# Optimization experiments

Measured on AMD Instinct MI355X. Metric: run time of the kernel, lower is better.

Reference implementation:

```python
import jax, jax.numpy as jnp
import numpy as np

B, N, HID = 8, 1024, 768
HEADS, LORA, HDIM = 12, 256, 64


def setup_inputs() -> dict:
    key = jax.random.key(0)
    k1, k2, k3 = jax.random.split(key, 3)
    hidden_states = jax.random.normal(k1, (B, N, HID), dtype=jnp.float32)
    attention_mask = jnp.ones((B, N), dtype=jnp.int32)
    # torch Linear weights are [out_features, in_features]
    Wt = jax.random.normal(k2, (HEADS, LORA, HID), dtype=jnp.float32) * (HID ** -0.5)
    Wa = jax.random.normal(k3, (HEADS, HDIM, LORA), dtype=jnp.float32) * (LORA ** -0.5)
    return {"hidden_states": hidden_states, "attention_mask": attention_mask,
            "Wt": Wt, "Wa": Wa}


def reference(hidden_states, attention_mask, Wt, Wa):
    # Per-head LoRA projection, batched over heads instead of a Python loop.
    # t: [b, h, n, head_dim]; repeat(1,1,3) in the original makes q = k = v = t.
    scale = hidden_states.shape[-1] ** -0.5  # input_dim ** -0.5
    t = jnp.einsum('bnd,hld->bhnl', hidden_states, Wt)
    t = jnp.einsum('bhnl,hel->bhne', t, Wa)
    scores = jnp.einsum('bhid,bhjd->bhij', t, t) * scale
    scores = jnp.where(attention_mask[:, None, None, :] == 0, -jnp.inf, scores)
    attn = jax.nn.softmax(scores, axis=-1)
    out = jnp.einsum('bhij,bhjd->bhid', attn, t)  # [b, h, n, d]
    b, h, n, d = out.shape
    return out.transpose(0, 2, 1, 3).reshape(b, n, h * d)
```

## Files before the change

### kernel.cpp

```cpp
#include <hip/hip_runtime.h>
#include <math.h>

#define BATCH 8
#define SEQ   1024
#define HID_  768
#define HEADS 12
#define LORA  256
#define HDIM  64

#define SCALE      0.03608439182435161f
#define SCALE_LOG2 0.05205863235888918f

typedef _Float16 f16_t;
typedef _Float16 f16x2 __attribute__((ext_vector_type(2)));
typedef _Float16 f16x4 __attribute__((ext_vector_type(4)));
typedef _Float16 f16x8 __attribute__((ext_vector_type(8)));
typedef float    f32x4 __attribute__((ext_vector_type(4)));

#define GLD16(g, l) __builtin_amdgcn_global_load_lds( \
    (const __attribute__((address_space(1))) void*)(g), \
    (__attribute__((address_space(3))) void*)(l), 16, 0, 0)

#define SW(c, r) ((((c) ^ ((r) & 7)) << 3))

#define N4_HS (BATCH * SEQ * HID_ / 4)

__global__ __launch_bounds__(256) void cvt_hs_kernel(
    const float4* __restrict__ hs, f16x4* __restrict__ hs_f)
{
    int stride = gridDim.x * blockDim.x;
    for (int i = blockIdx.x * blockDim.x + threadIdx.x; i < N4_HS; i += stride) {
        float4 v = hs[i];
        f16x4 o = {(f16_t)v.x, (f16_t)v.y, (f16_t)v.z, (f16_t)v.w};
        hs_f[i] = o;
    }
}

__global__ __launch_bounds__(256) void fuse_w_kernel(
    const float* __restrict__ Wt, const float* __restrict__ Wa,
    f16_t* __restrict__ w_f)
{
    __shared__ float s_a[64][68];
    __shared__ float s_b[64][36];

    const int bid = blockIdx.x;
    const int h   = bid / 24;
    const int d0  = (bid % 24) * 32;
    const int tid = threadIdx.x;
    const int ty  = tid >> 4;
    const int tx  = tid & 15;

    const float* wa_g = Wa + (size_t)h * HDIM * LORA;
    const float* wt_g = Wt + (size_t)h * LORA * HID_;

    float acc[4][2] = {{0.f, 0.f}, {0.f, 0.f}, {0.f, 0.f}, {0.f, 0.f}};

    for (int kc = 0; kc < 4; ++kc) {
        const int l0 = kc * 64;
        if (kc) __syncthreads();
        #pragma unroll
        for (int k = 0; k < 4; ++k) {
            int u = tid + k * 256;
            int r = u >> 4, c4 = (u & 15) * 4;
            *(float4*)&s_a[r][c4] = *(const float4*)&wa_g[(size_t)r * LORA + l0 + c4];
        }
        #pragma unroll
        for (int k = 0; k < 2; ++k) {
            int u = tid + k * 256;
            int r = u >> 3, c4 = (u & 7) * 4;
            *(float4*)&s_b[r][c4] = *(const float4*)&wt_g[(size_t)(l0 + r) * HID_ + d0 + c4];
        }
        __syncthreads();

        #pragma unroll 8
        for (int l = 0; l < 64; ++l) {
            float a0 = s_a[ty * 4 + 0][l];
            float a1 = s_a[ty * 4 + 1][l];
            float a2 = s_a[ty * 4 + 2][l];
            float a3 = s_a[ty * 4 + 3][l];
            float b0 = s_b[l][tx * 2 + 0];
            float b1 = s_b[l][tx * 2 + 1];
            acc[0][0] = fmaf(a0, b0, acc[0][0]); acc[0][1] = fmaf(a0, b1, acc[0][1]);
            acc[1][0] = fmaf(a1, b0, acc[1][0]); acc[1][1] = fmaf(a1, b1, acc[1][1]);
            acc[2][0] = fmaf(a2, b0, acc[2][0]); acc[2][1] = fmaf(a2, b1, acc[2][1]);
            acc[3][0] = fmaf(a3, b0, acc[3][0]); acc[3][1] = fmaf(a3, b1, acc[3][1]);
        }
    }

    f16_t* wg = w_f + (size_t)h * HDIM * HID_;
    #pragma unroll
    for (int i = 0; i < 4; ++i) {
        int e = ty * 4 + i;
        f16x2 o = {(f16_t)acc[i][0], (f16_t)acc[i][1]};
        *(f16x2*)&wg[(size_t)e * HID_ + d0 + tx * 2] = o;
    }
}

__global__ __launch_bounds__(256, 3) void gemm_t(
    const f16_t* __restrict__ hs_f, const f16_t* __restrict__ w_f,
    f16_t* __restrict__ t_f, f16_t* __restrict__ tT_f)
{
    __shared__ __attribute__((aligned(16))) char smem[49152];
    f16_t* s_hs = (f16_t*)smem;
    f16_t* s_wt = (f16_t*)(smem + 32768);
    f16_t* s_ob = (f16_t*)smem;

    const int bid   = blockIdx.x;
    const int ntile = bid & 7;
    const int h     = (bid >> 3) % HEADS;
    const int b     = bid / (8 * HEADS);
    const int n0    = ntile * 128;
    const int tid   = threadIdx.x;
    const int w     = tid >> 6;
    const int lane  = tid & 63;
    const int q     = lane >> 4;
    const int mr    = lane & 15;
    const int lrow  = lane >> 3;
    const int gswz  = (((lane & 7) ^ lrow) & 7) * 8;

    const f16_t* hs_g = hs_f + ((size_t)b * SEQ + n0) * HID_;
    const f16_t* w_g  = w_f + (size_t)h * HDIM * HID_;

    const f32x4 z4 = {0.f, 0.f, 0.f, 0.f};
    f32x4 acc[2][4];
    #pragma unroll
    for (int mt = 0; mt < 2; ++mt)
        #pragma unroll
        for (int et = 0; et < 4; ++et) acc[mt][et] = z4;

    auto STAGE = [&](int buf, int rd) {
        const int k0 = rd * 64;
        f16_t* sa = s_hs + buf * (128 * 64);
        f16_t* sb = s_wt + buf * (64 * 64);
        #pragma unroll
        for (int tt = 0; tt < 4; ++tt) {
            int r0 = w * 32 + tt * 8;
            GLD16(hs_g + (size_t)(r0 + lrow) * HID_ + k0 + gswz, sa + r0 * 64);
        }
        #pragma unroll
        for (int tt = 0; tt < 2; ++tt) {
            int r0 = w * 16 + tt * 8;
            GLD16(w_g + (size_t)(r0 + lrow) * HID_ + k0 + gswz, sb + r0 * 64);
        }
    };

    auto COMPUTE = [&](int buf) {
        const f16_t* sa = s_hs + buf * (128 * 64);
        const f16_t* sb = s_wt + buf * (64 * 64);
        #pragma unroll
        for (int ks = 0; ks < 2; ++ks) {
            f16x8 a_[2], b_[4];
            #pragma unroll
            for (int mt = 0; mt < 2; ++mt)
                a_[mt] = *(const f16x8*)(sa + (w * 32 + mt * 16 + mr) * 64 + SW(ks * 4 + q, mr));
            #pragma unroll
            for (int et = 0; et < 4; ++et)
                b_[et] = *(const f16x8*)(sb + (et * 16 + mr) * 64 + SW(ks * 4 + q, mr));
            #pragma unroll
            for (int mt = 0; mt < 2; ++mt)
                #pragma unroll
                for (int et = 0; et < 4; ++et)
                    acc[mt][et] = __builtin_amdgcn_mfma_f32_16x16x32_f16(a_[mt], b_[et], acc[mt][et], 0, 0, 0);
        }
    };

    STAGE(0, 0);
    __syncthreads();
    #pragma unroll 1
    for (int rr = 0; rr < 6; ++rr) {
        STAGE(1, 2 * rr + 1);
        COMPUTE(0);
        __syncthreads();
        if (rr < 5) STAGE(0, 2 * rr + 2);
        COMPUTE(1);
        __syncthreads();
    }

    #pragma unroll
    for (int mt = 0; mt < 2; ++mt) {
        #pragma unroll
        for (int et = 0; et < 4; ++et) {
            #pragma unroll
            for (int r = 0; r < 4; ++r) {
                int row = w * 32 + mt * 16 + q * 4 + r;
                int col = et * 16 + mr;
                s_ob[row * 72 + col] = (f16_t)acc[mt][et][r];
            }
        }
    }
    __syncthreads();

    f16_t* tg = t_f + (((size_t)b * HEADS + h) * SEQ + n0) * HDIM;
    #pragma unroll
    for (int k = 0; k < 4; ++k) {
        int u = tid + k * 256;
        int row = u >> 3, c8 = (u & 7) * 8;
        *(f16x8*)&tg[row * 64 + c8] = *(const f16x8*)&s_ob[row * 72 + c8];
    }
    f16_t* tTg = tT_f + ((size_t)b * HEADS + h) * SEQ * HDIM;
    #pragma unroll
    for (int k = 0; k < 4; ++k) {
        int u = tid + k * 256;
        int e = u & 63, n8 = (u >> 6) * 8;
        f16x8 v;
        #pragma unroll
        for (int j = 0; j < 8; ++j) v[j] = s_ob[(n8 + j) * 72 + e];
        *(f16x8*)&tTg[(size_t)e * SEQ + n0 + n8] = v;
    }
}

__global__ __launch_bounds__(256, 3) void attn_mfma(
    const f16_t* __restrict__ t_f, const f16_t* __restrict__ tT_f,
    const int* __restrict__ mask, float* __restrict__ out)
{
    __shared__ __attribute__((aligned(16))) char smem[34816];
    f16_t* s_k = (f16_t*)smem;
    f16_t* s_v = (f16_t*)(smem + 8192);
    f16_t* s_p = (f16_t*)(smem + 16384);
    float* s_m = (float*)smem;

    const int bid  = blockIdx.x;
    const int it   = bid & 7;
    const int h    = (bid >> 3) % HEADS;
    const int b    = bid / (8 * HEADS);
    const int i0   = it * 128;
    const int tid  = threadIdx.x;
    const int w    = tid >> 6;
    const int lane = tid & 63;
    const int q    = lane >> 4;
    const int mr   = lane & 15;
    const int lrow = lane >> 3;
    const int gswz = (((lane & 7) ^ lrow) & 7) * 8;
    const int ih   = w >> 1;
    const int jh   = w & 1;

    const size_t bh = ((size_t)b * HEADS + h) * SEQ * HDIM;
    const f16_t* th = t_f + bh;
    const f16_t* vh = tT_f + bh;
    const int* mk = mask + (size_t)b * SEQ;

    f16x8 qf[4][2];
    #pragma unroll
    for (int mt = 0; mt < 4; ++mt)
        #pragma unroll
        for (int ks = 0; ks < 2; ++ks) {
            f16x8 v = *(const f16x8*)(th + (size_t)(i0 + ih * 64 + mt * 16 + mr) * 64
                                      + ks * 32 + q * 8);
            #pragma unroll
            for (int j = 0; j < 8; ++j) v[j] = v[j] * (f16_t)SCALE_LOG2;
            qf[mt][ks] = v;
        }

    const f32x4 z4 = {0.f, 0.f, 0.f, 0.f};
    float l_[4] = {0.f, 0.f, 0.f, 0.f};
    f32x4 oT[4][4];
    #pragma unroll
    for (int mt = 0; mt < 4; ++mt)
        #pragma unroll
        for (int et = 0; et < 4; ++et) oT[mt][et] = z4;

    for (int jt6 = 0; jt6 < 16; ++jt6) {
        const int j0 = jt6 * 64;
        __syncthreads();
        #pragma unroll
        for (int t2 = 0; t2 < 2; ++t2) {
            int r0 = w * 16 + t2 * 8;
            GLD16(th + (size_t)(j0 + r0 + lrow) * 64 + gswz,  s_k + r0 * 64);
            GLD16(vh + (size_t)(r0 + lrow) * SEQ + j0 + gswz, s_v + r0 * 64);
        }
        __syncthreads();

        #pragma unroll
        for (int jt = 0; jt < 2; ++jt) {
            f32x4 st[4] = {z4, z4, z4, z4};
            #pragma unroll
            for (int ks = 0; ks < 2; ++ks) {
                f16x8 kf = *(const f16x8*)(s_k + (jh * 32 + jt * 16 + mr) * 64 + SW(ks * 4 + q, mr));
                #pragma unroll
                for (int mt = 0; mt < 4; ++mt)
                    st[mt] = __builtin_amdgcn_mfma_f32_16x16x32_f16(kf, qf[mt][ks], st[mt], 0, 0, 0);
            }
            int4 mv = *(const int4*)(mk + j0 + jh * 32 + jt * 16 + q * 4);
            #pragma unroll
            for (int mt = 0; mt < 4; ++mt) {
                float p0 = (mv.x == 0) ? 0.f : __builtin_amdgcn_exp2f(st[mt][0]);
                float p1 = (mv.y == 0) ? 0.f : __builtin_amdgcn_exp2f(st[mt][1]);
                float p2 = (mv.z == 0) ? 0.f : __builtin_amdgcn_exp2f(st[mt][2]);
                float p3 = (mv.w == 0) ? 0.f : __builtin_amdgcn_exp2f(st[mt][3]);
                l_[mt] += (p0 + p1) + (p2 + p3);
                f16x4 u4 = {(f16_t)p0, (f16_t)p1, (f16_t)p2, (f16_t)p3};
                *(f16x4*)&s_p[(ih * 64 + mt * 16 + mr) * 72 + jh * 32 + jt * 16 + q * 4] = u4;
            }
        }

        f16x8 pf[4];
        #pragma unroll
        for (int mt = 0; mt < 4; ++mt)
            pf[mt] = *(const f16x8*)(s_p + (ih * 64 + mt * 16 + mr) * 72 + jh * 32 + q * 8);
        #pragma unroll
        for (int et = 0; et < 4; ++et) {
            f16x8 vv = *(const f16x8*)(s_v + (et * 16 + mr) * 64 + SW(jh * 4 + q, mr));
            #pragma unroll
            for (int mt = 0; mt < 4; ++mt)
                oT[mt][et] = __builtin_amdgcn_mfma_f32_16x16x32_f16(vv, pf[mt], oT[mt][et], 0, 0, 0);
        }
    }

    #pragma unroll
    for (int mt = 0; mt < 4; ++mt) {
        l_[mt] += __shfl_xor(l_[mt], 16);
        l_[mt] += __shfl_xor(l_[mt], 32);
    }

    __syncthreads();
    if (jh == 1) {
        float* dst = s_m + ((size_t)ih * 64 + lane) * 68;
        #pragma unroll
        for (int mt = 0; mt < 4; ++mt) {
            #pragma unroll
            for (int et = 0; et < 4; ++et)
                *(f32x4*)&dst[(mt * 4 + et) * 4] = oT[mt][et];
            dst[64 + mt] = l_[mt];
        }
    }
    __syncthreads();
    if (jh == 0) {
        const float* src = s_m + ((size_t)ih * 64 + lane) * 68;
        #pragma unroll
        for (int mt = 0; mt < 4; ++mt) {
            float lt = l_[mt] + src[64 + mt];
            float inv = (lt > 0.f) ? 1.f / lt : 0.f;
            int n = i0 + ih * 64 + mt * 16 + mr;
            #pragma unroll
            for (int et = 0; et < 4; ++et) {
                f32x4 o2 = *(const f32x4*)&src[(mt * 4 + et) * 4];
                float4 v = {(oT[mt][et][0] + o2[0]) * inv, (oT[mt][et][1] + o2[1]) * inv,
                            (oT[mt][et][2] + o2[2]) * inv, (oT[mt][et][3] + o2[3]) * inv};
                *(float4*)&out[((size_t)b * SEQ + n) * (HEADS * HDIM) + h * HDIM + et * 16 + q * 4] = v;
            }
        }
    }
}

extern "C" void kernel_launch(void* const* d_in, const int* in_sizes, int n_in,
                              void* d_out, int out_size, void* d_ws, size_t ws_size,
                              hipStream_t stream) {
    const float* hs   = (const float*)d_in[0];
    const int*   mask = (const int*)d_in[1];
    const float* Wt   = (const float*)d_in[2];
    const float* Wa   = (const float*)d_in[3];
    float* out = (float*)d_out;

    char* ws = (char*)d_ws;
    f16_t* t_f  = (f16_t*)ws;
    f16_t* tT_f = (f16_t*)(ws + 12582912);
    f16_t* hs_f = (f16_t*)(ws + 25165824);
    f16_t* w_f  = (f16_t*)(ws + 37748736);

    cvt_hs_kernel<<<1024, 256, 0, stream>>>((const float4*)hs, (f16x4*)hs_f);

    fuse_w_kernel<<<HEADS * (HID_ / 32), 256, 0, stream>>>(Wt, Wa, w_f);

    gemm_t<<<BATCH * HEADS * (SEQ / 128), 256, 0, stream>>>(hs_f, w_f, t_f, tT_f);

    attn_mfma<<<BATCH * HEADS * (SEQ / 128), 256, 0, stream>>>(
        t_f, tT_f, mask, out);
}
```

Measured before the change: 157.8 us.

## Double-buffer K/V tiles in attention, merge prep kernels, swizzle P buffer

The hs conversion and weight-fusion kernels become one launch, with different blocks taking each role, which saves a launch and lets the two jobs overlap. The attention kernel now double-buffers its K/V LDS tiles, so the async global-to-LDS load of the next 64-column tile is issued before the current tile is processed, and it drops one barrier per iteration. The P staging buffer changes from padded rows to an XOR-swizzled layout, fp16 conversion uses packed cvt_pkrtz, and block order is remapped so consecutive blocks cover different batch-heads. LDS use grows from 34816 to 49152 bytes, which may limit how many blocks fit per CU. Packed round-toward-zero conversion also differs slightly in rounding from the previous casts.

```diff
diff --git a/kernel.cpp b/kernel.cpp
--- a/kernel.cpp
+++ b/kernel.cpp
@@ -25,28 +25,30 @@
 
 #define N4_HS (BATCH * SEQ * HID_ / 4)
 
-__global__ __launch_bounds__(256) void cvt_hs_kernel(
-    const float4* __restrict__ hs, f16x4* __restrict__ hs_f)
-{
-    int stride = gridDim.x * blockDim.x;
-    for (int i = blockIdx.x * blockDim.x + threadIdx.x; i < N4_HS; i += stride) {
-        float4 v = hs[i];
-        f16x4 o = {(f16_t)v.x, (f16_t)v.y, (f16_t)v.z, (f16_t)v.w};
-        hs_f[i] = o;
-    }
-}
-
-__global__ __launch_bounds__(256) void fuse_w_kernel(
-    const float* __restrict__ Wt, const float* __restrict__ Wa,
+__global__ __launch_bounds__(256) void prep_kernel(
+    const float4* __restrict__ hs, const float* __restrict__ Wt,
+    const float* __restrict__ Wa, f16x4* __restrict__ hs_f,
     f16_t* __restrict__ w_f)
 {
     __shared__ float s_a[64][68];
     __shared__ float s_b[64][36];
 
+    const int tid = threadIdx.x;
+
+    if (blockIdx.x >= 288) {
+        int i0 = (blockIdx.x - 288) * 256 + tid;
+        int stride = (gridDim.x - 288) * 256;
+        for (int i = i0; i < N4_HS; i += stride) {
+            float4 v = hs[i];
+            f16x4 o = {(f16_t)v.x, (f16_t)v.y, (f16_t)v.z, (f16_t)v.w};
+            hs_f[i] = o;
+        }
+        return;
+    }
+
     const int bid = blockIdx.x;
     const int h   = bid / 24;
     const int d0  = (bid % 24) * 32;
-    const int tid = threadIdx.x;
     const int ty  = tid >> 4;
     const int tx  = tid & 15;
 
@@ -213,16 +215,17 @@
     const f16_t* __restrict__ t_f, const f16_t* __restrict__ tT_f,
     const int* __restrict__ mask, float* __restrict__ out)
 {
-    __shared__ __attribute__((aligned(16))) char smem[34816];
+    __shared__ __attribute__((aligned(16))) char smem[49152];
     f16_t* s_k = (f16_t*)smem;
-    f16_t* s_v = (f16_t*)(smem + 8192);
-    f16_t* s_p = (f16_t*)(smem + 16384);
+    f16_t* s_v = (f16_t*)(smem + 16384);
+    f16_t* s_p = (f16_t*)(smem + 32768);
     float* s_m = (float*)smem;
 
     const int bid  = blockIdx.x;
-    const int it   = bid & 7;
-    const int h    = (bid >> 3) % HEADS;
-    const int b    = bid / (8 * HEADS);
+    const int bh   = bid % (BATCH * HEADS);
+    const int it   = bid / (BATCH * HEADS);
+    const int h    = bh % HEADS;
+    const int b    = bh / HEADS;
     const int i0   = it * 128;
     const int tid  = threadIdx.x;
     const int w    = tid >> 6;
@@ -234,9 +237,9 @@
     const int ih   = w >> 1;
     const int jh   = w & 1;
 
-    const size_t bh = ((size_t)b * HEADS + h) * SEQ * HDIM;
-    const f16_t* th = t_f + bh;
-    const f16_t* vh = tT_f + bh;
+    const size_t bh_off = ((size_t)b * HEADS + h) * SEQ * HDIM;
+    const f16_t* th = t_f + bh_off;
+    const f16_t* vh = tT_f + bh_off;
     const int* mk = mask + (size_t)b * SEQ;
 
     f16x8 qf[4][2];
@@ -259,28 +262,32 @@
         #pragma unroll
         for (int et = 0; et < 4; ++et) oT[mt][et] = z4;
 
-    for (int jt6 = 0; jt6 < 16; ++jt6) {
-        const int j0 = jt6 * 64;
-        __syncthreads();
+    auto STAGE = [&](int buf, int j0) {
+        f16_t* dk = s_k + buf * 4096;
+        f16_t* dv = s_v + buf * 4096;
         #pragma unroll
         for (int t2 = 0; t2 < 2; ++t2) {
             int r0 = w * 16 + t2 * 8;
-            GLD16(th + (size_t)(j0 + r0 + lrow) * 64 + gswz,  s_k + r0 * 64);
-            GLD16(vh + (size_t)(r0 + lrow) * SEQ + j0 + gswz, s_v + r0 * 64);
-        }
-        __syncthreads();
-
+            GLD16(th + (size_t)(j0 + r0 + lrow) * 64 + gswz,  dk + r0 * 64);
+            GLD16(vh + (size_t)(r0 + lrow) * SEQ + j0 + gswz, dv + r0 * 64);
+        }
+    };
+
+    auto PROCESS = [&](int buf, int j0) {
+        const f16_t* sk = s_k + buf * 4096;
+        const f16_t* sv = s_v + buf * 4096;
         #pragma unroll
         for (int jt = 0; jt < 2; ++jt) {
             f32x4 st[4] = {z4, z4, z4, z4};
             #pragma unroll
             for (int ks = 0; ks < 2; ++ks) {
-                f16x8 kf = *(const f16x8*)(s_k + (jh * 32 + jt * 16 + mr) * 64 + SW(ks * 4 + q, mr));
+                f16x8 kf = *(const f16x8*)(sk + (jh * 32 + jt * 16 + mr) * 64 + SW(ks * 4 + q, mr));
                 #pragma unroll
                 for (int mt = 0; mt < 4; ++mt)
                     st[mt] = __builtin_amdgcn_mfma_f32_16x16x32_f16(kf, qf[mt][ks], st[mt], 0, 0, 0);
             }
             int4 mv = *(const int4*)(mk + j0 + jh * 32 + jt * 16 + q * 4);
+            const int c8w = (jh * 4 + jt * 2 + (q >> 1)) ^ (mr & 7);
             #pragma unroll
             for (int mt = 0; mt < 4; ++mt) {
                 float p0 = (mv.x == 0) ? 0.f : __builtin_amdgcn_exp2f(st[mt][0]);
@@ -288,22 +295,37 @@
                 float p2 = (mv.z == 0) ? 0.f : __builtin_amdgcn_exp2f(st[mt][2]);
                 float p3 = (mv.w == 0) ? 0.f : __builtin_amdgcn_exp2f(st[mt][3]);
                 l_[mt] += (p0 + p1) + (p2 + p3);
-                f16x4 u4 = {(f16_t)p0, (f16_t)p1, (f16_t)p2, (f16_t)p3};
-                *(f16x4*)&s_p[(ih * 64 + mt * 16 + mr) * 72 + jh * 32 + jt * 16 + q * 4] = u4;
+                f16x2 lo = __builtin_bit_cast(f16x2, __builtin_amdgcn_cvt_pkrtz(p0, p1));
+                f16x2 hi = __builtin_bit_cast(f16x2, __builtin_amdgcn_cvt_pkrtz(p2, p3));
+                f16x4 u4 = __builtin_shufflevector(lo, hi, 0, 1, 2, 3);
+                int prow = ih * 64 + mt * 16 + mr;
+                *(f16x4*)&s_p[prow * 64 + (c8w << 3) + (q & 1) * 4] = u4;
             }
         }
-
         f16x8 pf[4];
+        const int c8r = (jh * 4 + q) ^ (mr & 7);
         #pragma unroll
         for (int mt = 0; mt < 4; ++mt)
-            pf[mt] = *(const f16x8*)(s_p + (ih * 64 + mt * 16 + mr) * 72 + jh * 32 + q * 8);
+            pf[mt] = *(const f16x8*)(s_p + (ih * 64 + mt * 16 + mr) * 64 + (c8r << 3));
         #pragma unroll
         for (int et = 0; et < 4; ++et) {
-            f16x8 vv = *(const f16x8*)(s_v + (et * 16 + mr) * 64 + SW(jh * 4 + q, mr));
+            f16x8 vv = *(const f16x8*)(sv + (et * 16 + mr) * 64 + SW(jh * 4 + q, mr));
             #pragma unroll
             for (int mt = 0; mt < 4; ++mt)
                 oT[mt][et] = __builtin_amdgcn_mfma_f32_16x16x32_f16(vv, pf[mt], oT[mt][et], 0, 0, 0);
         }
+    };
+
+    STAGE(0, 0);
+    __syncthreads();
+    #pragma unroll 1
+    for (int rr = 0; rr < 8; ++rr) {
+        STAGE(1, rr * 128 + 64);
+        PROCESS(0, rr * 128);
+        __syncthreads();
+        if (rr < 7) STAGE(0, rr * 128 + 128);
+        PROCESS(1, rr * 128 + 64);
+        __syncthreads();
     }
 
     #pragma unroll
@@ -312,7 +334,6 @@
         l_[mt] += __shfl_xor(l_[mt], 32);
     }
 
-    __syncthreads();
     if (jh == 1) {
         float* dst = s_m + ((size_t)ih * 64 + lane) * 68;
         #pragma unroll
@@ -357,9 +378,8 @@
     f16_t* hs_f = (f16_t*)(ws + 25165824);
     f16_t* w_f  = (f16_t*)(ws + 37748736);
 
-    cvt_hs_kernel<<<1024, 256, 0, stream>>>((const float4*)hs, (f16x4*)hs_f);
-
-    fuse_w_kernel<<<HEADS * (HID_ / 32), 256, 0, stream>>>(Wt, Wa, w_f);
+    prep_kernel<<<288 + 1024, 256, 0, stream>>>(
+        (const float4*)hs, Wt, Wa, (f16x4*)hs_f, w_f);
 
     gemm_t<<<BATCH * HEADS * (SEQ / 128), 256, 0, stream>>>(hs_f, w_f, t_f, tT_f);
 
```

Result: slower. 199.9 us (+26.7%).
